# Performance work log

Hardware: AMD Instinct MI355X
Metric: run time of the kernel (lower is better)

Reference implementation:

```python
import jax, jax.numpy as jnp
import numpy as np

# Standard NF4 quantization levels (bitsandbytes / QLoRA)
NF4_LEVELS = jnp.array([
    -1.0, -0.6961928009986877, -0.5250730514526367, -0.39491748809814453,
    -0.28444138169288635, -0.18477343022823334, -0.09105003625154495, 0.0,
    0.07958029955625534, 0.16093020141124725, 0.24611230194568634,
    0.33791524171829224, 0.44070982933044434, 0.5626170039176941,
    0.7229568362236023, 1.0], dtype=jnp.float32)

D_IN, D_OUT = 4096, 4096
BLOCK_SIZE = 64
N_VALS = D_IN * D_OUT              # 16_777_216 weights
N_BYTES = N_VALS // 2              # 2 nibbles per byte
NUM_BLOCKS = N_VALS // BLOCK_SIZE  # 262_144 per-block scales


def setup_inputs() -> dict:
    key = jax.random.key(0)
    k1, k2, k3, k4 = jax.random.split(key, 4)
    x = jax.random.normal(k1, (4, 2048, D_IN), dtype=jnp.float32)
    kernel_quantized = jax.random.randint(k2, (N_BYTES,), 0, 256, dtype=jnp.int32)
    kernel_scales = jax.random.uniform(k3, (NUM_BLOCKS,), dtype=jnp.float32)
    bias = jax.random.normal(k4, (D_OUT,), dtype=jnp.float32)
    return {"x": x, "kernel_quantized": kernel_quantized,
            "kernel_scales": kernel_scales, "bias": bias}


def nf4_dequantize(kernel_quantized, kernel_scales):
    # Unpack two 4-bit codes per byte (high nibble first), look up NF4 level,
    # scale per block of BLOCK_SIZE values, reshape to original kernel shape.
    high = (kernel_quantized >> 4) & 0xF
    low = kernel_quantized & 0xF
    codes = jnp.stack([high, low], axis=-1).reshape(-1)          # [N_VALS]
    vals = NF4_LEVELS[codes]                                     # [N_VALS]
    vals = vals.reshape(NUM_BLOCKS, BLOCK_SIZE) * kernel_scales[:, None]
    return vals.reshape(D_IN, D_OUT)                             # pad_length = 0


def reference(x, kernel_quantized, kernel_scales, bias):
    # Dense base-layer call on the dequantized kernel: x @ W + b
    W = nf4_dequantize(kernel_quantized, kernel_scales)
    out = jnp.einsum('bsd,de->bse', x, W) + bias
    return out.astype(jnp.float32)
```

## Files before the change

### kernel.cpp

```cpp
#include <hip/hip_runtime.h>
#include <hip/hip_bf16.h>
#include <stdint.h>

typedef __bf16 bf16x8 __attribute__((ext_vector_type(8)));
typedef float f32x4 __attribute__((ext_vector_type(4)));
typedef unsigned short ushort_t;
typedef ushort_t ushort8 __attribute__((ext_vector_type(8)));

#define GLDS16(g, l) __builtin_amdgcn_global_load_lds(                          \
    (const __attribute__((address_space(1))) void*)(g),                         \
    (__attribute__((address_space(3))) void*)(l), 16, 0, 0)

__device__ __constant__ float NF4_LUT_C[16] = {
    -1.0f, -0.6961928009986877f, -0.5250730514526367f, -0.39491748809814453f,
    -0.28444138169288635f, -0.18477343022823334f, -0.09105003625154495f, 0.0f,
    0.07958029955625534f, 0.16093020141124725f, 0.24611230194568634f,
    0.33791524171829224f, 0.44070982933044434f, 0.5626170039176941f,
    0.7229568362236023f, 1.0f};

__device__ inline ushort_t f32_to_bf16(float f) {
    uint32_t u = __builtin_bit_cast(uint32_t, f);
    u += 0x7FFFu + ((u >> 16) & 1u);
    return (ushort_t)(u >> 16);
}

__global__ __launch_bounds__(256) void cast_x_kernel(
    const float* __restrict__ x, ushort_t* __restrict__ xb)
{
    const int i = blockIdx.x * 256 + threadIdx.x;
    const float4* p = reinterpret_cast<const float4*>(x);
    float4 a = p[i * 2];
    float4 b = p[i * 2 + 1];
    ushort8 v;
    v[0] = f32_to_bf16(a.x); v[1] = f32_to_bf16(a.y);
    v[2] = f32_to_bf16(a.z); v[3] = f32_to_bf16(a.w);
    v[4] = f32_to_bf16(b.x); v[5] = f32_to_bf16(b.y);
    v[6] = f32_to_bf16(b.z); v[7] = f32_to_bf16(b.w);
    *reinterpret_cast<ushort8*>(xb + (size_t)i * 8) = v;
}

__global__ __launch_bounds__(256) void nf4_dequant_t_kernel(
    const int* __restrict__ q, const float* __restrict__ scales,
    ushort_t* __restrict__ Wt)
{
    __shared__ float lut[16];
    __shared__ ushort_t tile[64][65];
    const int t = threadIdx.x;
    if (t < 16) lut[t] = NF4_LUT_C[t];
    __syncthreads();

    const int nt = blockIdx.x & 63;
    const int kt = blockIdx.x >> 6;

    #pragma unroll
    for (int L = t; L < 512; L += 256) {
        const int r  = L >> 3;
        const int qd = L & 7;
        const int k  = kt * 64 + r;
        const int4 e4 = *reinterpret_cast<const int4*>(q + (size_t)k * 2048 + nt * 32 + qd * 4);
        const float s = scales[k * 64 + nt];
        const int nb = qd * 8;
        int bts[4] = {e4.x, e4.y, e4.z, e4.w};
        #pragma unroll
        for (int e = 0; e < 4; ++e) {
            const int byte = bts[e];
            tile[r][nb + e * 2]     = f32_to_bf16(lut[(byte >> 4) & 0xF] * s);
            tile[r][nb + e * 2 + 1] = f32_to_bf16(lut[byte & 0xF] * s);
        }
    }
    __syncthreads();

    const int nl = t >> 2;
    const int ks = (t & 3) * 16;
    ushort8 v0, v1;
    #pragma unroll
    for (int j = 0; j < 8; ++j) v0[j] = tile[ks + j][nl];
    #pragma unroll
    for (int j = 0; j < 8; ++j) v1[j] = tile[ks + 8 + j][nl];
    ushort_t* dst = Wt + (size_t)(nt * 64 + nl) * 4096 + kt * 64 + ks;
    *reinterpret_cast<ushort8*>(dst)     = v0;
    *reinterpret_cast<ushort8*>(dst + 8) = v1;
}


__device__ __forceinline__ void stage_tile(
    const ushort_t* __restrict__ A, const ushort_t* __restrict__ Bt,
    ushort_t (*Asb)[128 * 64], ushort_t (*Bsb)[128 * 64],
    int m0, int n0, int k0, int wid, int lane)
{
    const int lrow = lane >> 3;
    const int kswz = k0 + (((lane & 7) ^ lrow) << 3);
    #pragma unroll
    for (int r = 0; r < 4; ++r) {
        const int row = r * 64 + wid * 8;
        GLDS16(A + (size_t)(m0 + row + lrow) * 4096 + kswz,
               &Asb[r >> 1][(row & 127) * 64]);
    }
    #pragma unroll
    for (int r = 0; r < 4; ++r) {
        const int row = r * 64 + wid * 8;
        GLDS16(Bt + (size_t)(n0 + row + lrow) * 4096 + kswz,
               &Bsb[r >> 1][(row & 127) * 64]);
    }
}

__global__ __launch_bounds__(512, 2) void gemm_nf4_kernel(
    const ushort_t* __restrict__ A, const ushort_t* __restrict__ Bt,
    const float* __restrict__ bias, float* __restrict__ C)
{
    __shared__ __align__(16) ushort_t As[2][2][128 * 64];
    __shared__ __align__(16) ushort_t Bs[2][2][128 * 64];

    const int tid  = threadIdx.x;
    const int lane = tid & 63;
    const int wid  = tid >> 6;
    const int wr   = wid >> 2;
    const int wc   = wid & 3;
    const int ln15 = lane & 15;
    const int ln7  = lane & 7;
    const int lq   = lane >> 4;

    const int wg  = blockIdx.x;
    const int swz = (wg & 7) * 64 + (wg >> 3);
    const int m0  = (swz >> 4) * 256;
    const int n0  = (swz & 15) * 256;

    f32x4 acc[8][4];
    #pragma unroll
    for (int i = 0; i < 8; ++i)
        #pragma unroll
        for (int j = 0; j < 4; ++j)
            acc[i][j] = (f32x4){0.f, 0.f, 0.f, 0.f};

    stage_tile(A, Bt, As[0], Bs[0], m0, n0, 0,  wid, lane);
    stage_tile(A, Bt, As[1], Bs[1], m0, n0, 64, wid, lane);
    asm volatile("s_waitcnt vmcnt(8)" ::: "memory");
    __builtin_amdgcn_s_barrier();
    asm volatile("" ::: "memory");
    __builtin_amdgcn_sched_barrier(0);

    int p = 0;
    for (int t = 0; t < 64; ++t) {
        const ushort_t* Ah = As[p][wr];
        const ushort_t* Bh = Bs[p][wc >> 1];
        const int brow0 = (wc & 1) * 64;

        #pragma unroll
        for (int kk = 0; kk < 2; ++kk) {
            const int s = kk * 4 + lq;
            const int po = ((s ^ ln7) << 3);
            bf16x8 bf[4];
            #pragma unroll
            for (int j = 0; j < 4; ++j) {
                const int r = brow0 + j * 16 + ln15;
                bf[j] = *reinterpret_cast<const bf16x8*>(Bh + r * 64 + po);
            }
            #pragma unroll
            for (int mq = 0; mq < 2; ++mq) {
                bf16x8 af[4];
                #pragma unroll
                for (int i = 0; i < 4; ++i) {
                    const int r = mq * 64 + i * 16 + ln15;
                    af[i] = *reinterpret_cast<const bf16x8*>(Ah + r * 64 + po);
                }
                __builtin_amdgcn_s_setprio(1);
                #pragma unroll
                for (int i = 0; i < 4; ++i)
                    #pragma unroll
                    for (int j = 0; j < 4; ++j)
                        acc[mq * 4 + i][j] = __builtin_amdgcn_mfma_f32_16x16x32_bf16(
                            af[i], bf[j], acc[mq * 4 + i][j], 0, 0, 0);
                __builtin_amdgcn_s_setprio(0);
            }
        }

        asm volatile("" ::: "memory");
        __builtin_amdgcn_s_barrier();
        __builtin_amdgcn_sched_barrier(0);
        if (t + 2 < 64) {
            stage_tile(A, Bt, As[p], Bs[p], m0, n0, (t + 2) * 64, wid, lane);
            asm volatile("s_waitcnt vmcnt(8)" ::: "memory");
        } else {
            asm volatile("s_waitcnt vmcnt(0)" ::: "memory");
        }
        __builtin_amdgcn_s_barrier();
        asm volatile("" ::: "memory");
        __builtin_amdgcn_sched_barrier(0);
        p ^= 1;
    }

    const int crow0 = m0 + wr * 128 + lq * 4;
    const int ccol0 = n0 + wc * 64 + ln15;
    #pragma unroll
    for (int j = 0; j < 4; ++j) {
        const int c = ccol0 + j * 16;
        const float bv = bias[c];
        #pragma unroll
        for (int i = 0; i < 8; ++i) {
            const int r0 = crow0 + i * 16;
            #pragma unroll
            for (int v = 0; v < 4; ++v)
                C[(size_t)(r0 + v) * 4096 + c] = acc[i][j][v] + bv;
        }
    }
}

extern "C" void kernel_launch(void* const* d_in, const int* in_sizes, int n_in,
                              void* d_out, int out_size, void* d_ws, size_t ws_size,
                              hipStream_t stream) {
    const float* x      = (const float*)d_in[0];
    const int*   q      = (const int*)d_in[1];
    const float* scales = (const float*)d_in[2];
    const float* bias   = (const float*)d_in[3];
    float* out = (float*)d_out;

    ushort_t* xb = (ushort_t*)d_ws;
    ushort_t* Wt = (ushort_t*)((char*)d_ws + (size_t)64 * 1024 * 1024);

    cast_x_kernel<<<16384, 256, 0, stream>>>(x, xb);
    nf4_dequant_t_kernel<<<4096, 256, 0, stream>>>(q, scales, Wt);
    gemm_nf4_kernel<<<512, 512, 0, stream>>>(xb, Wt, bias, out);
}
```

Before: 333.9 us.

## Restructure GEMM main loop into 4-stage K=32 pipeline with split ping-pong phases

```diff
diff --git a/kernel.cpp b/kernel.cpp
--- a/kernel.cpp
+++ b/kernel.cpp
@@ -82,34 +82,12 @@
     *reinterpret_cast<ushort8*>(dst + 8) = v1;
 }
 
-
-__device__ __forceinline__ void stage_tile(
-    const ushort_t* __restrict__ A, const ushort_t* __restrict__ Bt,
-    ushort_t (*Asb)[128 * 64], ushort_t (*Bsb)[128 * 64],
-    int m0, int n0, int k0, int wid, int lane)
-{
-    const int lrow = lane >> 3;
-    const int kswz = k0 + (((lane & 7) ^ lrow) << 3);
-    #pragma unroll
-    for (int r = 0; r < 4; ++r) {
-        const int row = r * 64 + wid * 8;
-        GLDS16(A + (size_t)(m0 + row + lrow) * 4096 + kswz,
-               &Asb[r >> 1][(row & 127) * 64]);
-    }
-    #pragma unroll
-    for (int r = 0; r < 4; ++r) {
-        const int row = r * 64 + wid * 8;
-        GLDS16(Bt + (size_t)(n0 + row + lrow) * 4096 + kswz,
-               &Bsb[r >> 1][(row & 127) * 64]);
-    }
-}
-
 __global__ __launch_bounds__(512, 2) void gemm_nf4_kernel(
     const ushort_t* __restrict__ A, const ushort_t* __restrict__ Bt,
     const float* __restrict__ bias, float* __restrict__ C)
 {
-    __shared__ __align__(16) ushort_t As[2][2][128 * 64];
-    __shared__ __align__(16) ushort_t Bs[2][2][128 * 64];
+    __shared__ __align__(16) ushort_t As[4][256 * 32];
+    __shared__ __align__(16) ushort_t Bs[4][256 * 32];
 
     const int tid  = threadIdx.x;
     const int lane = tid & 63;
@@ -117,7 +95,6 @@
     const int wr   = wid >> 2;
     const int wc   = wid & 3;
     const int ln15 = lane & 15;
-    const int ln7  = lane & 7;
     const int lq   = lane >> 4;
 
     const int wg  = blockIdx.x;
@@ -125,6 +102,15 @@
     const int m0  = (swz >> 4) * 256;
     const int n0  = (swz & 15) * 256;
 
+    const int srow = wid * 16 + (lane >> 2);
+    const int scol = (lane & 3) * 8;
+    const ushort_t* gA0 = A  + (size_t)(m0 + srow) * 4096 + scol;
+    const ushort_t* gA1 = gA0 + (size_t)128 * 4096;
+    const ushort_t* gB0 = Bt + (size_t)(n0 + srow) * 4096 + scol;
+    const ushort_t* gB1 = gB0 + (size_t)128 * 4096;
+    const int ldsOff0 = (wid * 16) * 32;
+    const int ldsOff1 = (128 + wid * 16) * 32;
+
     f32x4 acc[8][4];
     #pragma unroll
     for (int i = 0; i < 8; ++i)
@@ -132,61 +118,82 @@
         for (int j = 0; j < 4; ++j)
             acc[i][j] = (f32x4){0.f, 0.f, 0.f, 0.f};
 
-    stage_tile(A, Bt, As[0], Bs[0], m0, n0, 0,  wid, lane);
-    stage_tile(A, Bt, As[1], Bs[1], m0, n0, 64, wid, lane);
+    const int rdA = (wr * 128 + ln15) * 32 + lq * 8;
+    const int rdB = (wc * 64  + ln15) * 32 + lq * 8;
+
+    #pragma unroll
+    for (int tt = 0; tt < 3; ++tt) {
+        const int kof = tt * 32;
+        GLDS16(gA0 + kof, &As[tt][ldsOff0]);
+        GLDS16(gA1 + kof, &As[tt][ldsOff1]);
+        GLDS16(gB0 + kof, &Bs[tt][ldsOff0]);
+        GLDS16(gB1 + kof, &Bs[tt][ldsOff1]);
+    }
     asm volatile("s_waitcnt vmcnt(8)" ::: "memory");
     __builtin_amdgcn_s_barrier();
     asm volatile("" ::: "memory");
-    __builtin_amdgcn_sched_barrier(0);
-
-    int p = 0;
-    for (int t = 0; t < 64; ++t) {
-        const ushort_t* Ah = As[p][wr];
-        const ushort_t* Bh = Bs[p][wc >> 1];
-        const int brow0 = (wc & 1) * 64;
-
-        #pragma unroll
-        for (int kk = 0; kk < 2; ++kk) {
-            const int s = kk * 4 + lq;
-            const int po = ((s ^ ln7) << 3);
-            bf16x8 bf[4];
+
+    for (int t = 0; t < 128; ++t) {
+        const int slot = t & 3;
+        const ushort_t* Asl = &As[slot][0];
+        const ushort_t* Bsl = &Bs[slot][0];
+
+        bf16x8 bf[4], af0[4], af1[4];
+        #pragma unroll
+        for (int j = 0; j < 4; ++j)
+            bf[j] = *reinterpret_cast<const bf16x8*>(Bsl + rdB + j * 16 * 32);
+        #pragma unroll
+        for (int i = 0; i < 4; ++i)
+            af0[i] = *reinterpret_cast<const bf16x8*>(Asl + rdA + i * 16 * 32);
+        if (t < 125) {
+            const int nslot = (t + 3) & 3;
+            const int kof = (t + 3) * 32;
+            GLDS16(gA0 + kof, &As[nslot][ldsOff0]);
+            GLDS16(gA1 + kof, &As[nslot][ldsOff1]);
+        }
+        asm volatile("" ::: "memory");
+        __builtin_amdgcn_s_barrier();
+        asm volatile("s_waitcnt lgkmcnt(0)" ::: "memory");
+        __builtin_amdgcn_sched_barrier(0);
+        __builtin_amdgcn_s_setprio(1);
+        #pragma unroll
+        for (int i = 0; i < 4; ++i)
             #pragma unroll
-            for (int j = 0; j < 4; ++j) {
-                const int r = brow0 + j * 16 + ln15;
-                bf[j] = *reinterpret_cast<const bf16x8*>(Bh + r * 64 + po);
-            }
+            for (int j = 0; j < 4; ++j)
+                acc[i][j] = __builtin_amdgcn_mfma_f32_16x16x32_bf16(
+                    af0[i], bf[j], acc[i][j], 0, 0, 0);
+        __builtin_amdgcn_s_setprio(0);
+        asm volatile("" ::: "memory");
+        __builtin_amdgcn_s_barrier();
+        asm volatile("" ::: "memory");
+
+        #pragma unroll
+        for (int i = 0; i < 4; ++i)
+            af1[i] = *reinterpret_cast<const bf16x8*>(Asl + rdA + (64 + i * 16) * 32);
+        if (t < 125) {
+            const int nslot = (t + 3) & 3;
+            const int kof = (t + 3) * 32;
+            GLDS16(gB0 + kof, &Bs[nslot][ldsOff0]);
+            GLDS16(gB1 + kof, &Bs[nslot][ldsOff1]);
+            asm volatile("s_waitcnt vmcnt(8)" ::: "memory");
+        } else if (t == 125) {
+            asm volatile("s_waitcnt vmcnt(0)" ::: "memory");
+        }
+        asm volatile("" ::: "memory");
+        __builtin_amdgcn_s_barrier();
+        asm volatile("s_waitcnt lgkmcnt(0)" ::: "memory");
+        __builtin_amdgcn_sched_barrier(0);
+        __builtin_amdgcn_s_setprio(1);
+        #pragma unroll
+        for (int i = 0; i < 4; ++i)
             #pragma unroll
-            for (int mq = 0; mq < 2; ++mq) {
-                bf16x8 af[4];
-                #pragma unroll
-                for (int i = 0; i < 4; ++i) {
-                    const int r = mq * 64 + i * 16 + ln15;
-                    af[i] = *reinterpret_cast<const bf16x8*>(Ah + r * 64 + po);
-                }
-                __builtin_amdgcn_s_setprio(1);
-                #pragma unroll
-                for (int i = 0; i < 4; ++i)
-                    #pragma unroll
-                    for (int j = 0; j < 4; ++j)
-                        acc[mq * 4 + i][j] = __builtin_amdgcn_mfma_f32_16x16x32_bf16(
-                            af[i], bf[j], acc[mq * 4 + i][j], 0, 0, 0);
-                __builtin_amdgcn_s_setprio(0);
-            }
-        }
-
-        asm volatile("" ::: "memory");
-        __builtin_amdgcn_s_barrier();
-        __builtin_amdgcn_sched_barrier(0);
-        if (t + 2 < 64) {
-            stage_tile(A, Bt, As[p], Bs[p], m0, n0, (t + 2) * 64, wid, lane);
-            asm volatile("s_waitcnt vmcnt(8)" ::: "memory");
-        } else {
-            asm volatile("s_waitcnt vmcnt(0)" ::: "memory");
-        }
-        __builtin_amdgcn_s_barrier();
-        asm volatile("" ::: "memory");
-        __builtin_amdgcn_sched_barrier(0);
-        p ^= 1;
+            for (int j = 0; j < 4; ++j)
+                acc[4 + i][j] = __builtin_amdgcn_mfma_f32_16x16x32_bf16(
+                    af1[i], bf[j], acc[4 + i][j], 0, 0, 0);
+        __builtin_amdgcn_s_setprio(0);
+        asm volatile("" ::: "memory");
+        __builtin_amdgcn_s_barrier();
+        asm volatile("" ::: "memory");
     }
 
     const int crow0 = m0 + wr * 128 + lq * 4;
```

New measurement: 327.7 us. No clear change (-1.8%).
